# Kernel optimization log

Measured on AMD Instinct MI355X. Metric: run time of the kernel, lower is better.

Reference implementation:

```python
import jax, jax.numpy as jnp
import numpy as np

N_NODES = 100000
N_EDGES = 1600000
N_HIDDEN = 128
EPS = 1e-12  # matches torch F.normalize default eps


def setup_inputs() -> dict:
    key = jax.random.key(0)
    k1, k2, k3, k4 = jax.random.split(key, 4)
    emb = jax.random.normal(k1, (N_NODES, N_HIDDEN), dtype=jnp.float32)
    src = jax.random.randint(k2, (N_EDGES,), 0, N_NODES, dtype=jnp.int64)
    dst = jax.random.randint(k3, (N_EDGES,), 0, N_NODES, dtype=jnp.int64)
    d = jnp.ones((N_HIDDEN,), dtype=jnp.float32)
    scale = jax.random.uniform(k4, (1,), dtype=jnp.float32)
    return {"emb": emb, "src": src, "dst": dst, "d": d, "scale": scale}


def reference(emb, src, dst, d, scale):
    # L2 normalize rows (torch F.normalize p=2, dim=1, eps=1e-12)
    norm = jnp.linalg.norm(emb, axis=1, keepdims=True)
    e = emb / jnp.maximum(norm, EPS)          # [N, H]
    ew = e * d                                 # diag scale, [N, H]
    # edge-wise u_dot_v: dot(ew[src], e[dst]) -> [E, 1]
    z = jnp.sum(ew[src] * e[dst], axis=-1, keepdims=True)
    return z * scale
```

## Files before the change

### kernel.cpp

```cpp
#include <hip/hip_runtime.h>

#define H 128
#define EPS 1e-12f

static __device__ __forceinline__ float bf_lo(unsigned int v) {
    return __uint_as_float(v << 16);
}
static __device__ __forceinline__ float bf_hi(unsigned int v) {
    return __uint_as_float(v & 0xFFFF0000u);
}
static __device__ __forceinline__ unsigned int f2bf_rne(float f) {
    unsigned int u = __float_as_uint(f);
    return (u + 0x7FFFu + ((u >> 16) & 1u)) >> 16;
}


__global__ void norm_quant_kernel(const float* __restrict__ emb,
                                  unsigned int* __restrict__ pool,
                                  int n_nodes) {
    int row = blockIdx.x * (blockDim.x >> 6) + (threadIdx.x >> 6);
    if (row >= n_nodes) return;
    int lane = threadIdx.x & 63;
    const float2* p = (const float2*)(emb + (size_t)row * H);
    float2 v = p[lane];
    float ss = v.x * v.x + v.y * v.y;
#pragma unroll
    for (int off = 32; off; off >>= 1) ss += __shfl_xor(ss, off);
    float inv = 1.0f / fmaxf(sqrtf(ss), EPS);
    unsigned int ua = f2bf_rne(v.x * inv);
    unsigned int ub = f2bf_rne(v.y * inv);
    pool[(size_t)row * 64 + lane] = ua | (ub << 16);
}

__global__ void edge_dot_bf16_kernel(const uint4* __restrict__ pool,
                                     const int* __restrict__ src,
                                     const int* __restrict__ dst,
                                     const float* __restrict__ d,
                                     const float* __restrict__ scale,
                                     float* __restrict__ out,
                                     int n_edges) {
    int lane = threadIdx.x & 63;
    int sub = lane >> 4;
    int q   = lane & 15;

    float4 d0 = ((const float4*)d)[q * 2];
    float4 d1 = ((const float4*)d)[q * 2 + 1];
    float sc = scale[0];

    int waveId = (blockIdx.x * blockDim.x + threadIdx.x) >> 6;
    int nWaves = (gridDim.x * blockDim.x) >> 6;

    for (int ebase = waveId * 4; ebase < n_edges; ebase += nWaves * 4) {
        int e = ebase + sub;
        bool valid = (e < n_edges);
        int s = valid ? src[e] : 0;
        int t = valid ? dst[e] : 0;

        uint4 va = pool[(size_t)s * 16 + q];
        uint4 vb = pool[(size_t)t * 16 + q];

        float p;
        p  = bf_lo(va.x) * d0.x * bf_lo(vb.x);
        p  = fmaf(bf_hi(va.x) * d0.y, bf_hi(vb.x), p);
        p  = fmaf(bf_lo(va.y) * d0.z, bf_lo(vb.y), p);
        p  = fmaf(bf_hi(va.y) * d0.w, bf_hi(vb.y), p);
        p  = fmaf(bf_lo(va.z) * d1.x, bf_lo(vb.z), p);
        p  = fmaf(bf_hi(va.z) * d1.y, bf_hi(vb.z), p);
        p  = fmaf(bf_lo(va.w) * d1.z, bf_lo(vb.w), p);
        p  = fmaf(bf_hi(va.w) * d1.w, bf_hi(vb.w), p);

        p += __shfl_xor(p, 1);
        p += __shfl_xor(p, 2);
        p += __shfl_xor(p, 4);
        p += __shfl_xor(p, 8);

        if (q == 0 && valid) out[e] = p * sc;
    }
}


__global__ void inv_norm_kernel(const float* __restrict__ emb,
                                float* __restrict__ inv,
                                int n_nodes) {
    int row = blockIdx.x * (blockDim.x >> 6) + (threadIdx.x >> 6);
    if (row >= n_nodes) return;
    int lane = threadIdx.x & 63;
    const float2* p = (const float2*)(emb + (size_t)row * H);
    float2 v = p[lane];
    float ss = v.x * v.x + v.y * v.y;
#pragma unroll
    for (int off = 32; off; off >>= 1) ss += __shfl_xor(ss, off);
    if (lane == 0) inv[row] = 1.0f / fmaxf(sqrtf(ss), EPS);
}

__global__ void edge_dot_kernel(const float* __restrict__ emb,
                                const float* __restrict__ inv,
                                const int* __restrict__ src,
                                const int* __restrict__ dst,
                                const float* __restrict__ d,
                                const float* __restrict__ scale,
                                float* __restrict__ out,
                                int n_edges) {
    int edge = blockIdx.x * (blockDim.x >> 6) + (threadIdx.x >> 6);
    if (edge >= n_edges) return;
    int lane = threadIdx.x & 63;
    int s = src[edge];
    int t = dst[edge];
    const float2* ps = (const float2*)(emb + (size_t)s * H);
    const float2* pt = (const float2*)(emb + (size_t)t * H);
    float2 dv = ((const float2*)d)[lane];
    float2 a = ps[lane];
    float2 b = pt[lane];
    float p = a.x * dv.x * b.x + a.y * dv.y * b.y;
#pragma unroll
    for (int off = 32; off; off >>= 1) p += __shfl_xor(p, off);
    if (lane == 0) out[edge] = p * inv[s] * inv[t] * scale[0];
}

extern "C" void kernel_launch(void* const* d_in, const int* in_sizes, int n_in,
                              void* d_out, int out_size, void* d_ws, size_t ws_size,
                              hipStream_t stream) {
    const float* emb   = (const float*)d_in[0];
    const int*   src   = (const int*)d_in[1];
    const int*   dst   = (const int*)d_in[2];
    const float* d     = (const float*)d_in[3];
    const float* scale = (const float*)d_in[4];
    float* out = (float*)d_out;

    int n_nodes = in_sizes[0] / H;
    int n_edges = in_sizes[1];

    size_t pool_bytes = (size_t)n_nodes * H * 2;

    if (ws_size >= pool_bytes) {
        unsigned int* pool = (unsigned int*)d_ws;

        int blocks1 = (n_nodes + 3) / 4;
        norm_quant_kernel<<<blocks1, 256, 0, stream>>>(emb, pool, n_nodes);

        int blocks2 = 2048;
        edge_dot_bf16_kernel<<<blocks2, 256, 0, stream>>>(
            (const uint4*)pool, src, dst, d, scale, out, n_edges);
    } else {
        float* inv = (float*)d_ws;
        int blocks1 = (n_nodes + 3) / 4;
        inv_norm_kernel<<<blocks1, 256, 0, stream>>>(emb, inv, n_nodes);
        int blocks2 = (n_edges + 3) / 4;
        edge_dot_kernel<<<blocks2, 256, 0, stream>>>(emb, inv, src, dst, d,
                                                     scale, out, n_edges);
    }
}
```

Before: 124.1 us.

## Process 16 edges per wave with 8 lanes each and nontemporal streaming

```diff
diff --git a/kernel.cpp b/kernel.cpp
--- a/kernel.cpp
+++ b/kernel.cpp
@@ -14,6 +14,18 @@
     return (u + 0x7FFFu + ((u >> 16) & 1u)) >> 16;
 }
 
+static __device__ __forceinline__ float dot8(uint4 a, uint4 b,
+                                             float4 d0, float4 d1, float p) {
+    p = fmaf(bf_lo(a.x) * d0.x, bf_lo(b.x), p);
+    p = fmaf(bf_hi(a.x) * d0.y, bf_hi(b.x), p);
+    p = fmaf(bf_lo(a.y) * d0.z, bf_lo(b.y), p);
+    p = fmaf(bf_hi(a.y) * d0.w, bf_hi(b.y), p);
+    p = fmaf(bf_lo(a.z) * d1.x, bf_lo(b.z), p);
+    p = fmaf(bf_hi(a.z) * d1.y, bf_hi(b.z), p);
+    p = fmaf(bf_lo(a.w) * d1.z, bf_lo(b.w), p);
+    p = fmaf(bf_hi(a.w) * d1.w, bf_hi(b.w), p);
+    return p;
+}
 
 __global__ void norm_quant_kernel(const float* __restrict__ emb,
                                   unsigned int* __restrict__ pool,
@@ -21,14 +33,15 @@
     int row = blockIdx.x * (blockDim.x >> 6) + (threadIdx.x >> 6);
     if (row >= n_nodes) return;
     int lane = threadIdx.x & 63;
-    const float2* p = (const float2*)(emb + (size_t)row * H);
-    float2 v = p[lane];
-    float ss = v.x * v.x + v.y * v.y;
+    const float* p = emb + (size_t)row * H + lane * 2;
+    float vx = __builtin_nontemporal_load(p);
+    float vy = __builtin_nontemporal_load(p + 1);
+    float ss = vx * vx + vy * vy;
 #pragma unroll
     for (int off = 32; off; off >>= 1) ss += __shfl_xor(ss, off);
     float inv = 1.0f / fmaxf(sqrtf(ss), EPS);
-    unsigned int ua = f2bf_rne(v.x * inv);
-    unsigned int ub = f2bf_rne(v.y * inv);
+    unsigned int ua = f2bf_rne(vx * inv);
+    unsigned int ub = f2bf_rne(vy * inv);
     pool[(size_t)row * 64 + lane] = ua | (ub << 16);
 }
 
@@ -40,41 +53,61 @@
                                      float* __restrict__ out,
                                      int n_edges) {
     int lane = threadIdx.x & 63;
-    int sub = lane >> 4;
-    int q   = lane & 15;
+    int sub  = lane >> 3;
+    int q    = lane & 7;
 
-    float4 d0 = ((const float4*)d)[q * 2];
-    float4 d1 = ((const float4*)d)[q * 2 + 1];
+    float4 dv0 = ((const float4*)d)[q * 4 + 0];
+    float4 dv1 = ((const float4*)d)[q * 4 + 1];
+    float4 dv2 = ((const float4*)d)[q * 4 + 2];
+    float4 dv3 = ((const float4*)d)[q * 4 + 3];
     float sc = scale[0];
 
     int waveId = (blockIdx.x * blockDim.x + threadIdx.x) >> 6;
     int nWaves = (gridDim.x * blockDim.x) >> 6;
+    int last = n_edges - 1;
 
-    for (int ebase = waveId * 4; ebase < n_edges; ebase += nWaves * 4) {
-        int e = ebase + sub;
-        bool valid = (e < n_edges);
-        int s = valid ? src[e] : 0;
-        int t = valid ? dst[e] : 0;
+    for (int ebase = waveId * 16; ebase < n_edges; ebase += nWaves * 16) {
+        int e0 = ebase + sub;
+        int e1 = ebase + 8 + sub;
+        bool w0 = (e0 < n_edges);
+        bool w1 = (e1 < n_edges);
+        int c0 = w0 ? e0 : last;
+        int c1 = w1 ? e1 : last;
 
-        uint4 va = pool[(size_t)s * 16 + q];
-        uint4 vb = pool[(size_t)t * 16 + q];
+        int s0 = __builtin_nontemporal_load(src + c0);
+        int t0 = __builtin_nontemporal_load(dst + c0);
+        int s1 = __builtin_nontemporal_load(src + c1);
+        int t1 = __builtin_nontemporal_load(dst + c1);
 
-        float p;
-        p  = bf_lo(va.x) * d0.x * bf_lo(vb.x);
-        p  = fmaf(bf_hi(va.x) * d0.y, bf_hi(vb.x), p);
-        p  = fmaf(bf_lo(va.y) * d0.z, bf_lo(vb.y), p);
-        p  = fmaf(bf_hi(va.y) * d0.w, bf_hi(vb.y), p);
-        p  = fmaf(bf_lo(va.z) * d1.x, bf_lo(vb.z), p);
-        p  = fmaf(bf_hi(va.z) * d1.y, bf_hi(vb.z), p);
-        p  = fmaf(bf_lo(va.w) * d1.z, bf_lo(vb.w), p);
-        p  = fmaf(bf_hi(va.w) * d1.w, bf_hi(vb.w), p);
+        const uint4* pa0 = pool + (size_t)s0 * 16 + q * 2;
+        const uint4* pb0 = pool + (size_t)t0 * 16 + q * 2;
+        const uint4* pa1 = pool + (size_t)s1 * 16 + q * 2;
+        const uint4* pb1 = pool + (size_t)t1 * 16 + q * 2;
+        uint4 a00 = pa0[0];
+        uint4 a01 = pa0[1];
+        uint4 b00 = pb0[0];
+        uint4 b01 = pb0[1];
+        uint4 a10 = pa1[0];
+        uint4 a11 = pa1[1];
+        uint4 b10 = pb1[0];
+        uint4 b11 = pb1[1];
 
-        p += __shfl_xor(p, 1);
-        p += __shfl_xor(p, 2);
-        p += __shfl_xor(p, 4);
-        p += __shfl_xor(p, 8);
+        float p0 = dot8(a00, b00, dv0, dv1, 0.0f);
+        p0 = dot8(a01, b01, dv2, dv3, p0);
+        float p1 = dot8(a10, b10, dv0, dv1, 0.0f);
+        p1 = dot8(a11, b11, dv2, dv3, p1);
 
-        if (q == 0 && valid) out[e] = p * sc;
+        p0 += __shfl_xor(p0, 1);
+        p1 += __shfl_xor(p1, 1);
+        p0 += __shfl_xor(p0, 2);
+        p1 += __shfl_xor(p1, 2);
+        p0 += __shfl_xor(p0, 4);
+        p1 += __shfl_xor(p1, 4);
+
+        if (q == 0) {
+            if (w0) __builtin_nontemporal_store(p0 * sc, out + e0);
+            if (w1) __builtin_nontemporal_store(p1 * sc, out + e1);
+        }
     }
 }
 
```

After: 125.7 us. About the same (+1.3%).
